# Kernel tuning notes

Hardware: AMD Instinct MI355X
Metric: run time of the kernel (lower is better)

## Reference

```python
import jax, jax.numpy as jnp
import numpy as np

CUBOID = (2, 7, 7)
SHIFT = (1, 3, 3)
NUM_HEADS = 4
LN_EPS = 1e-5


def _cuboid_reorder(data, cs):
    # (B,T,H,W,C) -> (B, num_cuboids, cuboid_volume, C), strategy = ('l','l','l')
    B, T, H, W, C = data.shape
    bt, bh, bw = cs
    d = data.reshape(B, T // bt, bt, H // bh, bh, W // bw, bw, C)
    d = d.transpose(0, 1, 3, 5, 2, 4, 6, 7)
    return d.reshape(B, (T // bt) * (H // bh) * (W // bw), bt * bh * bw, C)


def _cuboid_reorder_reverse(data, cs, shape):
    T, H, W = shape
    bt, bh, bw = cs
    B, _, _, C = data.shape
    d = data.reshape(B, T // bt, H // bh, W // bw, bt, bh, bw, C)
    d = d.transpose(0, 1, 4, 2, 5, 3, 6, 7)
    return d.reshape(B, T, H, W, C)


def _compute_attn_mask(shape, cs, ss):
    # Shift-window mask; no padding needed (dims divisible by cuboid), so the
    # data mask is all-ones and the mask is just the shift-region equality mask.
    T, H, W = shape
    shift_mask = np.zeros((1, T, H, W, 1), np.float32)
    cnt = 0
    for t in (slice(-cs[0]), slice(-cs[0], -ss[0]), slice(-ss[0], None)):
        for h in (slice(-cs[1]), slice(-cs[1], -ss[1]), slice(-ss[1], None)):
            for w in (slice(-cs[2]), slice(-cs[2], -ss[2]), slice(-ss[2], None)):
                shift_mask[:, t, h, w, :] = cnt
                cnt += 1
    sm = _cuboid_reorder(shift_mask, cs)[0, :, :, 0]  # (num_cuboids, vol)
    attn_mask = (sm[:, None, :] - sm[:, :, None]) == 0  # (num_cuboids, vol, vol)
    return jnp.asarray(attn_mask)


def setup_inputs() -> dict:
    key = jax.random.key(0)
    k1, k2, k3 = jax.random.split(key, 3)
    B, T, H, W, C = 2, 16, 56, 56, 128
    return {
        "x": jax.random.normal(k1, (B, T, H, W, C), jnp.float32),
        "gamma": jnp.ones((C,), jnp.float32),
        "beta": jnp.zeros((C,), jnp.float32),
        "w_qkv": jax.random.normal(k2, (C, 3 * C), jnp.float32) * 0.05,
        "w_proj": jax.random.normal(k3, (C, C), jnp.float32) * 0.05,
        "b_proj": jnp.zeros((C,), jnp.float32),
    }


def reference(x, gamma, beta, w_qkv, w_proj, b_proj):
    B, T, H, W, C = x.shape
    hd = C // NUM_HEADS
    scale = hd ** -0.5

    # pre-norm (torch LayerNorm, biased variance)
    mu = jnp.mean(x, axis=-1, keepdims=True)
    var = jnp.var(x, axis=-1, keepdims=True)
    xn = (x - mu) * jax.lax.rsqrt(var + LN_EPS) * gamma + beta

    # shift + cuboid reorder
    shifted = jnp.roll(xn, shift=(-SHIFT[0], -SHIFT[1], -SHIFT[2]), axis=(1, 2, 3))
    r = _cuboid_reorder(shifted, CUBOID)  # (B, nc, vol, C)
    nc, vol = r.shape[1], r.shape[2]

    qkv = (r @ w_qkv).reshape(B, nc, vol, 3, NUM_HEADS, hd)
    q = qkv[..., 0, :, :] * scale  # (B, nc, vol, h, d)
    k = qkv[..., 1, :, :]
    v = qkv[..., 2, :, :]

    attn_score = jnp.einsum("bnihd,bnjhd->bhnij", q, k)  # (B, h, nc, vol, vol)
    mask = _compute_attn_mask((T, H, W), CUBOID, SHIFT)  # (nc, vol, vol)
    attn_score = jnp.where(mask[None, None], attn_score, jnp.float32(-1e18))
    attn = jax.nn.softmax(attn_score, axis=-1) * mask[None, None]

    out = jnp.einsum("bhnij,bnjhd->bnihd", attn, v).reshape(B, nc, vol, C)
    out = out @ w_proj + b_proj

    out = _cuboid_reorder_reverse(out, CUBOID, (T, H, W))
    out = jnp.roll(out, shift=SHIFT, axis=(1, 2, 3))
    return out
```

## Files before the change

### kernel.cpp

```cpp
#include <hip/hip_runtime.h>

typedef short s16x8 __attribute__((ext_vector_type(8)));
typedef float f32x4_t __attribute__((ext_vector_type(4)));

#define VOL 98
#define VPAD 112
#define CH 128
#define NWV 7
#define NTH (NWV * 64)
#define MASKNEG -1e9f

struct Smem {
  unsigned short bufA[VPAD * CH];
  unsigned short vt[CH * CH];
  unsigned short pst[NWV][16 * 64];
  unsigned int catbits[27][4];
  int cat[VPAD];
  int gidx[VPAD];
};

__device__ __forceinline__ unsigned short f2bf(float f) {
  unsigned int u = __float_as_uint(f);
  unsigned int r = u + 0x7FFFu + ((u >> 16) & 1u);
  return (unsigned short)(r >> 16);
}
__device__ __forceinline__ unsigned int pk2(float a, float b) {
#if __has_builtin(__builtin_amdgcn_perm)
  return __builtin_amdgcn_perm(__float_as_uint(b) + 0x8000u,
                               __float_as_uint(a) + 0x8000u,
                               0x07060302u);
#else
  return (unsigned int)f2bf(a) | ((unsigned int)f2bf(b) << 16);
#endif
}
__device__ __forceinline__ int swz(int row, int colEl, int strideB) {
  return (row * strideB + colEl * 2) ^ ((row & 7) << 4);
}
__device__ __forceinline__ s16x8 ldsRd(const unsigned short* buf, int row, int colEl, int strideB) {
  return *(const s16x8*)((const char*)buf + swz(row, colEl, strideB));
}
__device__ __forceinline__ void ldsWr64(unsigned short* buf, int row, int colEl, int strideB,
                                        unsigned int lo, unsigned int hi) {
  unsigned long long v = (unsigned long long)lo | ((unsigned long long)hi << 32);
  *(unsigned long long*)((char*)buf + swz(row, colEl, strideB)) = v;
}
__device__ __forceinline__ s16x8 ldsRdP(const unsigned short* buf, int row, int colEl, int strideB) {
  const char* p = (const char*)buf;
  unsigned long long lo = *(const unsigned long long*)(p + swz(row, colEl, strideB));
  unsigned long long hi = *(const unsigned long long*)(p + swz(row, colEl, strideB) + 8);
  union { unsigned long long q[2]; s16x8 v; } u;
  u.q[0] = lo; u.q[1] = hi;
  return u.v;
}
__device__ __forceinline__ void ldsWr128(unsigned short* buf, int row, int colEl, int strideB, uint4 v) {
  *(uint4*)((char*)buf + swz(row, colEl, strideB)) = v;
}
__device__ __forceinline__ s16x8 u4cast(unsigned a, unsigned b, unsigned c, unsigned d) {
  union { uint4 u; s16x8 v; } cv;
  cv.u = make_uint4(a, b, c, d);
  return cv.v;
}

__global__ void prepack_weights(const float* __restrict__ wqkv,
                                const float* __restrict__ wproj,
                                unsigned short* __restrict__ dst) {
  const float QSCALE = (float)(0.17677669529663687 * 1.4426950408889634);
  int lane = threadIdx.x;
  int blk = blockIdx.x;
  if (blk < 96) {
    int ct = blk >> 2, ks = blk & 3;
    int r0 = ks * 32 + ((lane >> 4) << 3);
    int col = ct * 16 + (lane & 15);
    float scl = (ct < 8) ? QSCALE : 1.0f;
    unsigned short* d = dst + (((size_t)(ct * 4 + ks) * 64 + lane) * 8);
#pragma unroll
    for (int j = 0; j < 8; ++j) d[j] = f2bf(wqkv[(size_t)(r0 + j) * 384 + col] * scl);
  } else {
    int bb = blk - 96;
    int ct = bb >> 2, ks = bb & 3;
    int r0 = ks * 32 + ((lane >> 4) << 3);
    int col = ct * 16 + (lane & 15);
    unsigned short* d = dst + 49152 + (((size_t)(ct * 4 + ks) * 64 + lane) * 8);
#pragma unroll
    for (int j = 0; j < 8; ++j) d[j] = f2bf(wproj[(size_t)(r0 + j) * 128 + col]);
  }
}

__global__ __launch_bounds__(NTH, 4) void fused_cuboid_attn(
    const float* __restrict__ x, const float* __restrict__ gamma,
    const float* __restrict__ beta, const float* __restrict__ bproj,
    const unsigned short* __restrict__ wfrag, float* __restrict__ out) {
  __shared__ Smem s;
  const int tid = threadIdx.x;
  const int lane = tid & 63;
  const int itw = tid >> 6;
  const int l15 = lane & 15;
  const int lg = lane >> 4;
  const int lg4 = lg * 4;
  const int lg8 = lg * 8;
  const int bid = blockIdx.x;
  const int b = bid >> 9;
  const int n = bid & 511;
  const int nt = n >> 6, nh = (n >> 3) & 7, nw = n & 7;
  const int srcA = (2 * (lg & 1)) * 16 + l15;
  const int srcB = (2 * (lg & 1) + 1) * 16 + l15;
  const bool hiT = (lg >> 1) != 0;

  const int grp = tid >> 4;
  const int l = tid & 15;
  float4 xv[4][2];
  int giv[4], catv[4];
#pragma unroll
  for (int it2 = 0; it2 < 4; ++it2) {
    int i = grp + it2 * 28;
    if (i < VOL) {
      int dt = (i >= 49) ? 1 : 0;
      int rem = i - dt * 49;
      int dh = (rem * 37) >> 8;
      int dw = rem - dh * 7;
      int t = nt * 2 + dt, h = nh * 7 + dh, w = nw * 7 + dw;
      int ts = (t + 1) & 15;
      int hs = h + 3; if (hs >= 56) hs -= 56;
      int ws2 = w + 3; if (ws2 >= 56) ws2 -= 56;
      int gi = ((b * 16 + ts) * 56 + hs) * 56 + ws2;
      const float* xp = x + (size_t)gi * CH + l * 8;
      xv[it2][0] = *(const float4*)(xp);
      xv[it2][1] = *(const float4*)(xp + 4);
      giv[it2] = gi;
      int tc = (t < 14) ? 0 : ((t < 15) ? 1 : 2);
      int hc = (h < 49) ? 0 : ((h < 53) ? 1 : 2);
      int wc = (w < 49) ? 0 : ((w < 53) ? 1 : 2);
      catv[it2] = tc * 9 + hc * 3 + wc;
    }
  }

  {
    uint4 z = make_uint4(0, 0, 0, 0);
    uint4* pv = (uint4*)s.vt;
    for (int i = tid; i < 2048; i += NTH) pv[i] = z;
    if (tid < 224) ((uint4*)(s.bufA + 98 * CH))[tid] = z;
    if (tid < 27) ((uint4*)s.catbits)[tid] = z;
    if (tid >= NTH - (VPAD - VOL)) s.cat[VOL + tid - (NTH - (VPAD - VOL))] = -1;
  }
  __syncthreads();

  {
    const float4 g0 = *(const float4*)(gamma + l * 8);
    const float4 g1 = *(const float4*)(gamma + l * 8 + 4);
    const float4 be0 = *(const float4*)(beta + l * 8);
    const float4 be1 = *(const float4*)(beta + l * 8 + 4);
#pragma unroll
    for (int it2 = 0; it2 < 4; ++it2) {
      int i = grp + it2 * 28;
      if (i < VOL) {
        float4 v0 = xv[it2][0];
        float4 v1 = xv[it2][1];
        float sum = v0.x + v0.y + v0.z + v0.w + v1.x + v1.y + v1.z + v1.w;
        float ssq = v0.x * v0.x + v0.y * v0.y + v0.z * v0.z + v0.w * v0.w +
                    v1.x * v1.x + v1.y * v1.y + v1.z * v1.z + v1.w * v1.w;
#pragma unroll
        for (int d = 1; d < 16; d <<= 1) {
          sum += __shfl_xor(sum, d);
          ssq += __shfl_xor(ssq, d);
        }
        float mean = sum * (1.0f / 128.0f);
        float var = ssq * (1.0f / 128.0f) - mean * mean;
        float rstd = rsqrtf(var + 1e-5f);
        uint4 pkv;
        pkv.x = pk2((v0.x - mean) * rstd * g0.x + be0.x, (v0.y - mean) * rstd * g0.y + be0.y);
        pkv.y = pk2((v0.z - mean) * rstd * g0.z + be0.z, (v0.w - mean) * rstd * g0.w + be0.w);
        pkv.z = pk2((v1.x - mean) * rstd * g1.x + be1.x, (v1.y - mean) * rstd * g1.y + be1.y);
        pkv.w = pk2((v1.z - mean) * rstd * g1.z + be1.z, (v1.w - mean) * rstd * g1.w + be1.w);
        ldsWr128(s.bufA, i, l * 8, 256, pkv);
        if (l == 0) {
          s.cat[i] = catv[it2];
          s.gidx[i] = giv[it2];
          atomicOr(&s.catbits[catv[it2]][i >> 5], 1u << (i & 31));
        }
      }
    }
  }
  __syncthreads();

  s16x8 xf[4];
#pragma unroll
  for (int ks = 0; ks < 4; ++ks) xf[ks] = ldsRd(s.bufA, itw * 16 + l15, ks * 32 + lg8, 256);
  asm volatile("" ::: "memory");

  unsigned qp[8][2];
  {
#pragma unroll
    for (int ct = 0; ct < 24; ++ct) {
      const unsigned short* wf = wfrag + ((size_t)ct * 2048 + (size_t)lane * 8);
      s16x8 wv[4];
#pragma unroll
      for (int ks = 0; ks < 4; ++ks) wv[ks] = *(const s16x8*)(wf + ks * 512);
      f32x4_t acc = {0.f, 0.f, 0.f, 0.f};
      if (ct < 16) {
#pragma unroll
        for (int ks = 0; ks < 4; ++ks)
          acc = __builtin_amdgcn_mfma_f32_16x16x32_bf16(wv[ks], xf[ks], acc, 0, 0, 0);
        if (ct < 8) {
          qp[ct][0] = pk2(acc[0], acc[1]);
          qp[ct][1] = pk2(acc[2], acc[3]);
        } else {
          ldsWr64(s.bufA, itw * 16 + l15, (ct - 8) * 16 + lg4, 256,
                  pk2(acc[0], acc[1]), pk2(acc[2], acc[3]));
        }
      } else {
#pragma unroll
        for (int ks = 0; ks < 4; ++ks)
          acc = __builtin_amdgcn_mfma_f32_16x16x32_bf16(xf[ks], wv[ks], acc, 0, 0, 0);
        ldsWr64(s.vt, (ct - 16) * 16 + l15, itw * 16 + lg4, 256,
                pk2(acc[0], acc[1]), pk2(acc[2], acc[3]));
      }
    }
  }
  __syncthreads();

  unsigned oreg[4][4];
  {
    unsigned short* ps = s.pst[itw];
    const int q = itw * 16 + l15;
    int cq = s.cat[q]; if (cq < 0) cq = 0;
    const uint4 mwv = *(const uint4*)&s.catbits[cq][0];
    f32x4_t cm[7];
#pragma unroll
    for (int jt = 0; jt < 7; ++jt) {
      unsigned mword = ((jt >> 1) == 0) ? mwv.x : ((jt >> 1) == 1) ? mwv.y
                      : ((jt >> 1) == 2) ? mwv.z : mwv.w;
#pragma unroll
      for (int r = 0; r < 4; ++r)
        cm[jt][r] = ((mword >> ((jt & 1) * 16 + lg4 + r)) & 1u) ? 0.f : MASKNEG;
    }
#pragma unroll
    for (int hh = 0; hh < 4; ++hh) {
      unsigned a0 = __shfl(qp[2 * hh][0], srcA), b0 = __shfl(qp[2 * hh + 1][0], srcA);
      unsigned a1 = __shfl(qp[2 * hh][1], srcA), b1 = __shfl(qp[2 * hh + 1][1], srcA);
      unsigned a2 = __shfl(qp[2 * hh][0], srcB), b2 = __shfl(qp[2 * hh + 1][0], srcB);
      unsigned a3 = __shfl(qp[2 * hh][1], srcB), b3 = __shfl(qp[2 * hh + 1][1], srcB);
      s16x8 qa = u4cast(hiT ? b0 : a0, hiT ? b1 : a1, hiT ? b2 : a2, hiT ? b3 : a3);
      f32x4_t sc[7];
#pragma unroll
      for (int jt = 0; jt < 7; ++jt) {
        s16x8 kb = ldsRd(s.bufA, jt * 16 + l15, hh * 32 + lg8, 256);
        sc[jt] = __builtin_amdgcn_mfma_f32_16x16x32_bf16(kb, qa, cm[jt], 0, 0, 0);
      }
      float s0 = 0.f, s1 = 0.f, s2 = 0.f, s3 = 0.f;
#pragma unroll
      for (int jt = 0; jt < 7; ++jt) {
        float p0 = exp2f(sc[jt][0]);
        float p1 = exp2f(sc[jt][1]);
        float p2 = exp2f(sc[jt][2]);
        float p3 = exp2f(sc[jt][3]);
        sc[jt][0] = p0; sc[jt][1] = p1; sc[jt][2] = p2; sc[jt][3] = p3;
        s0 += p0; s1 += p1; s2 += p2; s3 += p3;
      }
      float ssum = (s0 + s1) + (s2 + s3);
      ssum += __shfl_xor(ssum, 16);
      ssum += __shfl_xor(ssum, 32);
      float rinv = 1.0f / ssum;
      f32x4_t o0 = {0.f, 0.f, 0.f, 0.f}, o1 = {0.f, 0.f, 0.f, 0.f};
#pragma unroll
      for (int jt = 0; jt < 4; ++jt)
        ldsWr64(ps, l15, jt * 16 + lg4, 128, pk2(sc[jt][0], sc[jt][1]), pk2(sc[jt][2], sc[jt][3]));
#pragma unroll
      for (int ks = 0; ks < 2; ++ks) {
        s16x8 pa = ldsRdP(ps, l15, ks * 32 + lg8, 128);
        s16x8 v0 = ldsRd(s.vt, hh * 32 + l15, ks * 32 + lg8, 256);
        s16x8 v1 = ldsRd(s.vt, hh * 32 + 16 + l15, ks * 32 + lg8, 256);
        o0 = __builtin_amdgcn_mfma_f32_16x16x32_bf16(v0, pa, o0, 0, 0, 0);
        o1 = __builtin_amdgcn_mfma_f32_16x16x32_bf16(v1, pa, o1, 0, 0, 0);
      }
#pragma unroll
      for (int jt = 4; jt < 7; ++jt)
        ldsWr64(ps, l15, (jt - 4) * 16 + lg4, 128, pk2(sc[jt][0], sc[jt][1]), pk2(sc[jt][2], sc[jt][3]));
      ldsWr64(ps, l15, 48 + lg4, 128, 0u, 0u);
#pragma unroll
      for (int ks = 0; ks < 2; ++ks) {
        s16x8 pa = ldsRdP(ps, l15, ks * 32 + lg8, 128);
        s16x8 v0 = ldsRd(s.vt, hh * 32 + l15, (2 + ks) * 32 + lg8, 256);
        s16x8 v1 = ldsRd(s.vt, hh * 32 + 16 + l15, (2 + ks) * 32 + lg8, 256);
        o0 = __builtin_amdgcn_mfma_f32_16x16x32_bf16(v0, pa, o0, 0, 0, 0);
        o1 = __builtin_amdgcn_mfma_f32_16x16x32_bf16(v1, pa, o1, 0, 0, 0);
      }
      oreg[hh][0] = pk2(o0[0] * rinv, o0[1] * rinv);
      oreg[hh][1] = pk2(o0[2] * rinv, o0[3] * rinv);
      oreg[hh][2] = pk2(o1[0] * rinv, o1[1] * rinv);
      oreg[hh][3] = pk2(o1[2] * rinv, o1[3] * rinv);
    }
  }

  {
    s16x8 of[4];
#pragma unroll
    for (int hh = 0; hh < 4; ++hh) {
      unsigned a0 = __shfl(oreg[hh][0], srcA), a2 = __shfl(oreg[hh][2], srcA);
      unsigned a1 = __shfl(oreg[hh][1], srcA), a3 = __shfl(oreg[hh][3], srcA);
      unsigned c0 = __shfl(oreg[hh][0], srcB), c2 = __shfl(oreg[hh][2], srcB);
      unsigned c1 = __shfl(oreg[hh][1], srcB), c3 = __shfl(oreg[hh][3], srcB);
      of[hh] = u4cast(hiT ? a2 : a0, hiT ? a3 : a1, hiT ? c2 : c0, hiT ? c3 : c1);
    }
    const unsigned short* wp = wfrag + 49152;
    const int row = itw * 16 + l15;
    const bool valid = row < VOL;
    const size_t gbase = valid ? (size_t)s.gidx[row] * CH : 0;
#pragma unroll
    for (int ct = 0; ct < 8; ++ct) {
      const unsigned short* wf = wp + ((size_t)ct * 2048 + (size_t)lane * 8);
      float4 b4 = *(const float4*)(bproj + ct * 16 + lg4);
      f32x4_t acc = {b4.x, b4.y, b4.z, b4.w};
#pragma unroll
      for (int ks = 0; ks < 4; ++ks) {
        s16x8 wv = *(const s16x8*)(wf + ks * 512);
        acc = __builtin_amdgcn_mfma_f32_16x16x32_bf16(wv, of[ks], acc, 0, 0, 0);
      }
      if (valid) {
        float4 res;
        res.x = acc[0]; res.y = acc[1]; res.z = acc[2]; res.w = acc[3];
        *(float4*)(out + gbase + ct * 16 + lg4) = res;
      }
    }
  }
}

extern "C" void kernel_launch(void* const* d_in, const int* in_sizes, int n_in,
                              void* d_out, int out_size, void* d_ws, size_t ws_size,
                              hipStream_t stream) {
  const float* x = (const float*)d_in[0];
  const float* gamma = (const float*)d_in[1];
  const float* beta = (const float*)d_in[2];
  const float* wqkv = (const float*)d_in[3];
  const float* wproj = (const float*)d_in[4];
  const float* bproj = (const float*)d_in[5];
  float* out = (float*)d_out;
  unsigned short* wsf = (unsigned short*)d_ws;
  (void)in_sizes; (void)n_in; (void)out_size; (void)ws_size;

  prepack_weights<<<128, 64, 0, stream>>>(wqkv, wproj, wsf);
  fused_cuboid_attn<<<1024, NTH, 0, stream>>>(x, gamma, beta, bproj, wsf, out);
}
```

Before: 69.77 us.

## Restructure QKV projection so each wave computes a K/V column tile across all rows

Instead of each wave projecting its own 16 rows through all 24 weight tiles, each wave now loads one K and one V weight tile once and sweeps all 7 row tiles, reading the normalized inputs from LDS. The remaining eighth K/V tile is still computed per wave from its own rows. The aim is to cut global weight-fragment loads per wave. The cost is extra LDS reads of activations, K results held in registers, and an added barrier before K is written back, since bufA is overwritten in place.

```diff
diff --git a/kernel.cpp b/kernel.cpp
--- a/kernel.cpp
+++ b/kernel.cpp
@@ -185,36 +185,80 @@
   s16x8 xf[4];
 #pragma unroll
   for (int ks = 0; ks < 4; ++ks) xf[ks] = ldsRd(s.bufA, itw * 16 + l15, ks * 32 + lg8, 256);
-  asm volatile("" ::: "memory");
 
   unsigned qp[8][2];
-  {
-#pragma unroll
-    for (int ct = 0; ct < 24; ++ct) {
-      const unsigned short* wf = wfrag + ((size_t)ct * 2048 + (size_t)lane * 8);
-      s16x8 wv[4];
-#pragma unroll
-      for (int ks = 0; ks < 4; ++ks) wv[ks] = *(const s16x8*)(wf + ks * 512);
+#pragma unroll
+  for (int ct = 0; ct < 8; ++ct) {
+    const unsigned short* wf = wfrag + ((size_t)ct * 2048 + (size_t)lane * 8);
+    f32x4_t acc = {0.f, 0.f, 0.f, 0.f};
+#pragma unroll
+    for (int ks = 0; ks < 4; ++ks) {
+      s16x8 wv = *(const s16x8*)(wf + ks * 512);
+      acc = __builtin_amdgcn_mfma_f32_16x16x32_bf16(wv, xf[ks], acc, 0, 0, 0);
+    }
+    qp[ct][0] = pk2(acc[0], acc[1]);
+    qp[ct][1] = pk2(acc[2], acc[3]);
+  }
+
+  unsigned kreg[8][2];
+  {
+    const unsigned short* wfk = wfrag + ((size_t)(8 + itw) * 2048 + (size_t)lane * 8);
+    s16x8 wvk[4];
+#pragma unroll
+    for (int ks = 0; ks < 4; ++ks) wvk[ks] = *(const s16x8*)(wfk + ks * 512);
+#pragma unroll
+    for (int it = 0; it < 7; ++it) {
       f32x4_t acc = {0.f, 0.f, 0.f, 0.f};
-      if (ct < 16) {
-#pragma unroll
-        for (int ks = 0; ks < 4; ++ks)
-          acc = __builtin_amdgcn_mfma_f32_16x16x32_bf16(wv[ks], xf[ks], acc, 0, 0, 0);
-        if (ct < 8) {
-          qp[ct][0] = pk2(acc[0], acc[1]);
-          qp[ct][1] = pk2(acc[2], acc[3]);
-        } else {
-          ldsWr64(s.bufA, itw * 16 + l15, (ct - 8) * 16 + lg4, 256,
-                  pk2(acc[0], acc[1]), pk2(acc[2], acc[3]));
-        }
-      } else {
-#pragma unroll
-        for (int ks = 0; ks < 4; ++ks)
-          acc = __builtin_amdgcn_mfma_f32_16x16x32_bf16(xf[ks], wv[ks], acc, 0, 0, 0);
-        ldsWr64(s.vt, (ct - 16) * 16 + l15, itw * 16 + lg4, 256,
-                pk2(acc[0], acc[1]), pk2(acc[2], acc[3]));
-      }
-    }
+#pragma unroll
+      for (int ks = 0; ks < 4; ++ks) {
+        s16x8 a = ldsRd(s.bufA, it * 16 + l15, ks * 32 + lg8, 256);
+        acc = __builtin_amdgcn_mfma_f32_16x16x32_bf16(wvk[ks], a, acc, 0, 0, 0);
+      }
+      kreg[it][0] = pk2(acc[0], acc[1]);
+      kreg[it][1] = pk2(acc[2], acc[3]);
+    }
+    const unsigned short* wfk2 = wfrag + ((size_t)15 * 2048 + (size_t)lane * 8);
+    f32x4_t acc = {0.f, 0.f, 0.f, 0.f};
+#pragma unroll
+    for (int ks = 0; ks < 4; ++ks) {
+      s16x8 wv = *(const s16x8*)(wfk2 + ks * 512);
+      acc = __builtin_amdgcn_mfma_f32_16x16x32_bf16(wv, xf[ks], acc, 0, 0, 0);
+    }
+    kreg[7][0] = pk2(acc[0], acc[1]);
+    kreg[7][1] = pk2(acc[2], acc[3]);
+  }
+  {
+    const unsigned short* wfv = wfrag + ((size_t)(16 + itw) * 2048 + (size_t)lane * 8);
+    s16x8 wvv[4];
+#pragma unroll
+    for (int ks = 0; ks < 4; ++ks) wvv[ks] = *(const s16x8*)(wfv + ks * 512);
+#pragma unroll
+    for (int it = 0; it < 7; ++it) {
+      f32x4_t acc = {0.f, 0.f, 0.f, 0.f};
+#pragma unroll
+      for (int ks = 0; ks < 4; ++ks) {
+        s16x8 a = ldsRd(s.bufA, it * 16 + l15, ks * 32 + lg8, 256);
+        acc = __builtin_amdgcn_mfma_f32_16x16x32_bf16(a, wvv[ks], acc, 0, 0, 0);
+      }
+      ldsWr64(s.vt, itw * 16 + l15, it * 16 + lg4, 256,
+              pk2(acc[0], acc[1]), pk2(acc[2], acc[3]));
+    }
+    const unsigned short* wfv2 = wfrag + ((size_t)23 * 2048 + (size_t)lane * 8);
+    f32x4_t acc = {0.f, 0.f, 0.f, 0.f};
+#pragma unroll
+    for (int ks = 0; ks < 4; ++ks) {
+      s16x8 wv = *(const s16x8*)(wfv2 + ks * 512);
+      acc = __builtin_amdgcn_mfma_f32_16x16x32_bf16(xf[ks], wv, acc, 0, 0, 0);
+    }
+    ldsWr64(s.vt, 112 + l15, itw * 16 + lg4, 256, pk2(acc[0], acc[1]), pk2(acc[2], acc[3]));
+  }
+  __syncthreads();
+
+  {
+#pragma unroll
+    for (int it = 0; it < 7; ++it)
+      ldsWr64(s.bufA, it * 16 + l15, itw * 16 + lg4, 256, kreg[it][0], kreg[it][1]);
+    ldsWr64(s.bufA, itw * 16 + l15, 112 + lg4, 256, kreg[7][0], kreg[7][1]);
   }
   __syncthreads();
 
```

New measurement: 74.28 us. 1.06x slower.

## Remap LayerNorm rows per wave to drop block barriers and shared index tables

Applied to the files above, without the earlier changes.

Each wave now loads and normalizes exactly the 16 rows it later reads as its MFMA A-fragment. That lets the two __syncthreads around the LayerNorm stage be replaced with a compiler fence. The shared cat/gidx tables are gone: category and global index are recomputed arithmetically where needed. The catbits mask and the zero padding of vt and bufA are built by wave 6 after the QKV stage, ahead of the single remaining barrier. The cost is redundant integer index math and a serial 32-iteration bit-building loop on one wave.

```diff
diff --git a/kernel.cpp b/kernel.cpp
--- a/kernel.cpp
+++ b/kernel.cpp
@@ -15,8 +15,6 @@
   unsigned short vt[CH * CH];
   unsigned short pst[NWV][16 * 64];
   unsigned int catbits[27][4];
-  int cat[VPAD];
-  int gidx[VPAD];
 };
 
 __device__ __forceinline__ unsigned short f2bf(float f) {
@@ -59,6 +57,28 @@
   union { uint4 u; s16x8 v; } cv;
   cv.u = make_uint4(a, b, c, d);
   return cv.v;
+}
+__device__ __forceinline__ int cat_of(int i, int nt, int nh, int nw) {
+  int dt = (i >= 49) ? 1 : 0;
+  int rem = i - dt * 49;
+  int dh = (rem * 37) >> 8;
+  int dw = rem - dh * 7;
+  int t = nt * 2 + dt, h = nh * 7 + dh, w = nw * 7 + dw;
+  int tc = (t < 14) ? 0 : ((t < 15) ? 1 : 2);
+  int hc = (h < 49) ? 0 : ((h < 53) ? 1 : 2);
+  int wc = (w < 49) ? 0 : ((w < 53) ? 1 : 2);
+  return tc * 9 + hc * 3 + wc;
+}
+__device__ __forceinline__ int gidx_of(int i, int b, int nt, int nh, int nw) {
+  int dt = (i >= 49) ? 1 : 0;
+  int rem = i - dt * 49;
+  int dh = (rem * 37) >> 8;
+  int dw = rem - dh * 7;
+  int t = nt * 2 + dt, h = nh * 7 + dh, w = nw * 7 + dw;
+  int ts = (t + 1) & 15;
+  int hs = h + 3; if (hs >= 56) hs -= 56;
+  int ws2 = w + 3; if (ws2 >= 56) ws2 -= 56;
+  return ((b * 16 + ts) * 56 + hs) * 56 + ws2;
 }
 
 __global__ void prepack_weights(const float* __restrict__ wqkv,
@@ -106,55 +126,28 @@
   const int srcB = (2 * (lg & 1) + 1) * 16 + l15;
   const bool hiT = (lg >> 1) != 0;
 
-  const int grp = tid >> 4;
-  const int l = tid & 15;
   float4 xv[4][2];
-  int giv[4], catv[4];
-#pragma unroll
-  for (int it2 = 0; it2 < 4; ++it2) {
-    int i = grp + it2 * 28;
+#pragma unroll
+  for (int k = 0; k < 4; ++k) {
+    int i = itw * 16 + lg * 4 + k;
     if (i < VOL) {
-      int dt = (i >= 49) ? 1 : 0;
-      int rem = i - dt * 49;
-      int dh = (rem * 37) >> 8;
-      int dw = rem - dh * 7;
-      int t = nt * 2 + dt, h = nh * 7 + dh, w = nw * 7 + dw;
-      int ts = (t + 1) & 15;
-      int hs = h + 3; if (hs >= 56) hs -= 56;
-      int ws2 = w + 3; if (ws2 >= 56) ws2 -= 56;
-      int gi = ((b * 16 + ts) * 56 + hs) * 56 + ws2;
-      const float* xp = x + (size_t)gi * CH + l * 8;
-      xv[it2][0] = *(const float4*)(xp);
-      xv[it2][1] = *(const float4*)(xp + 4);
-      giv[it2] = gi;
-      int tc = (t < 14) ? 0 : ((t < 15) ? 1 : 2);
-      int hc = (h < 49) ? 0 : ((h < 53) ? 1 : 2);
-      int wc = (w < 49) ? 0 : ((w < 53) ? 1 : 2);
-      catv[it2] = tc * 9 + hc * 3 + wc;
+      const float* xp = x + (size_t)gidx_of(i, b, nt, nh, nw) * CH + l15 * 8;
+      xv[k][0] = *(const float4*)(xp);
+      xv[k][1] = *(const float4*)(xp + 4);
     }
   }
 
   {
-    uint4 z = make_uint4(0, 0, 0, 0);
-    uint4* pv = (uint4*)s.vt;
-    for (int i = tid; i < 2048; i += NTH) pv[i] = z;
-    if (tid < 224) ((uint4*)(s.bufA + 98 * CH))[tid] = z;
-    if (tid < 27) ((uint4*)s.catbits)[tid] = z;
-    if (tid >= NTH - (VPAD - VOL)) s.cat[VOL + tid - (NTH - (VPAD - VOL))] = -1;
-  }
-  __syncthreads();
-
-  {
-    const float4 g0 = *(const float4*)(gamma + l * 8);
-    const float4 g1 = *(const float4*)(gamma + l * 8 + 4);
-    const float4 be0 = *(const float4*)(beta + l * 8);
-    const float4 be1 = *(const float4*)(beta + l * 8 + 4);
-#pragma unroll
-    for (int it2 = 0; it2 < 4; ++it2) {
-      int i = grp + it2 * 28;
+    const float4 g0 = *(const float4*)(gamma + l15 * 8);
+    const float4 g1 = *(const float4*)(gamma + l15 * 8 + 4);
+    const float4 be0 = *(const float4*)(beta + l15 * 8);
+    const float4 be1 = *(const float4*)(beta + l15 * 8 + 4);
+#pragma unroll
+    for (int k = 0; k < 4; ++k) {
+      int i = itw * 16 + lg * 4 + k;
       if (i < VOL) {
-        float4 v0 = xv[it2][0];
-        float4 v1 = xv[it2][1];
+        float4 v0 = xv[k][0];
+        float4 v1 = xv[k][1];
         float sum = v0.x + v0.y + v0.z + v0.w + v1.x + v1.y + v1.z + v1.w;
         float ssq = v0.x * v0.x + v0.y * v0.y + v0.z * v0.z + v0.w * v0.w +
                     v1.x * v1.x + v1.y * v1.y + v1.z * v1.z + v1.w * v1.w;
@@ -171,16 +164,20 @@
         pkv.y = pk2((v0.z - mean) * rstd * g0.z + be0.z, (v0.w - mean) * rstd * g0.w + be0.w);
         pkv.z = pk2((v1.x - mean) * rstd * g1.x + be1.x, (v1.y - mean) * rstd * g1.y + be1.y);
         pkv.w = pk2((v1.z - mean) * rstd * g1.z + be1.z, (v1.w - mean) * rstd * g1.w + be1.w);
-        ldsWr128(s.bufA, i, l * 8, 256, pkv);
-        if (l == 0) {
-          s.cat[i] = catv[it2];
-          s.gidx[i] = giv[it2];
-          atomicOr(&s.catbits[catv[it2]][i >> 5], 1u << (i & 31));
-        }
-      }
-    }
-  }
-  __syncthreads();
+        ldsWr128(s.bufA, i, l15 * 8, 256, pkv);
+      }
+    }
+  }
+  if (itw == 6) {
+    uint4 z = make_uint4(0, 0, 0, 0);
+    uint4* px = (uint4*)(s.bufA + 98 * CH);
+#pragma unroll
+    for (int r = 0; r < 4; ++r) {
+      int idx = lane + r * 64;
+      if (idx < 224) px[idx] = z;
+    }
+  }
+  asm volatile("" ::: "memory");
 
   s16x8 xf[4];
 #pragma unroll
@@ -216,13 +213,31 @@
       }
     }
   }
+  if (itw == 6) {
+    uint4 z = make_uint4(0, 0, 0, 0);
+#pragma unroll
+    for (int r = 0; r < 2; ++r) {
+      int row = lane + r * 64;
+      ldsWr128(s.vt, row, 112, 256, z);
+      ldsWr128(s.vt, row, 120, 256, z);
+    }
+    for (int wIdx = lane; wIdx < 108; wIdx += 64) {
+      int c = wIdx >> 2, wi = wIdx & 3;
+      unsigned bits = 0;
+      for (int bbit = 0; bbit < 32; ++bbit) {
+        int j = wi * 32 + bbit;
+        if (j < VOL && cat_of(j, nt, nh, nw) == c) bits |= (1u << bbit);
+      }
+      s.catbits[c][wi] = bits;
+    }
+  }
   __syncthreads();
 
   unsigned oreg[4][4];
   {
     unsigned short* ps = s.pst[itw];
     const int q = itw * 16 + l15;
-    int cq = s.cat[q]; if (cq < 0) cq = 0;
+    const int cq = (q < VOL) ? cat_of(q, nt, nh, nw) : 0;
     const uint4 mwv = *(const uint4*)&s.catbits[cq][0];
     f32x4_t cm[7];
 #pragma unroll
@@ -304,7 +319,7 @@
     const unsigned short* wp = wfrag + 49152;
     const int row = itw * 16 + l15;
     const bool valid = row < VOL;
-    const size_t gbase = valid ? (size_t)s.gidx[row] * CH : 0;
+    const size_t gbase = valid ? (size_t)gidx_of(row, b, nt, nh, nw) * CH : 0;
 #pragma unroll
     for (int ct = 0; ct < 8; ++ct) {
       const unsigned short* wf = wp + ((size_t)ct * 2048 + (size_t)lane * 8);
```

Result: slower. 75.09 us (+7.6%).
